# Optimization experiments

Measured on AMD Instinct MI355X. Metric: run time of the kernel, lower is better.

The kernel has to match this reference:

```python
import jax, jax.numpy as jnp
import numpy as np

MU = 0.02
BINS = 30
LOSS_WEIGHT = 1.0
REWEIGHT = 1.0


def setup_inputs() -> dict:
    key = jax.random.key(0)
    k1, k2, k3 = jax.random.split(key, 3)
    B, C = 4194304, 4
    pred = jax.random.normal(k1, (B, C), dtype=jnp.float32)
    target = jax.random.normal(k2, (B, C), dtype=jnp.float32)
    label_weight = jax.random.uniform(k3, (B, C), dtype=jnp.float32)
    return {"pred": pred, "target": target, "label_weight": label_weight}


def reference(pred, target, label_weight):
    mu = jnp.float32(MU)
    diff = pred - target
    # smooth-L1-like (ASL1) loss
    loss = jnp.sqrt(diff * diff + mu * mu) - mu
    # gradient norm g = |d / sqrt(mu^2 + d^2)| in [0, 1); detached in torch
    g = jax.lax.stop_gradient(jnp.abs(diff) * jax.lax.rsqrt(mu * mu + diff * diff))
    valid = label_weight > 0
    # tot comes from .item() in torch -> constant w.r.t. autodiff
    tot = jax.lax.stop_gradient(jnp.maximum(jnp.sum(label_weight), 1.0))
    # edges[i] = i/bins, edges[-1] = 1000 -> bin index = clip(floor(g*bins))
    idx = jnp.clip((g * BINS).astype(jnp.int32), 0, BINS - 1)
    counts = jax.ops.segment_sum(
        valid.astype(jnp.float32).ravel(), idx.ravel(), num_segments=BINS
    )  # [BINS] number of valid samples per gradient-density bin
    n = jnp.sum(counts > 0)  # number of non-empty bins
    weights = jnp.where(valid, tot / jnp.maximum(counts[idx], 1.0), 0.0)
    weights = weights / jnp.maximum(n, 1).astype(jnp.float32)
    weights = jax.lax.stop_gradient(weights)
    loss = jnp.sum(loss * weights * REWEIGHT) / tot
    return loss * LOSS_WEIGHT
```

## Files before the change

kernel.cpp:

```cpp
#include <hip/hip_runtime.h>

#define MU_F    0.02f
#define MU2_F   4.0e-4f
#define TSLOW_F 6.2e-3f
#define BINS    30
#define ROWS    62
#define THREADS 256
#define NBLK    2048

__device__ __forceinline__ void ghmr_elem(float pj, float tj, float wj,
                                          float& sumAll, float& cntAll,
                                          float* s_sum, unsigned int* s_cnt)
{
    float d    = pj - tj;
    float d2   = fmaf(d, d, MU2_F);
    float loss = sqrtf(d2) - MU_F;
    bool valid = wj > 0.0f;
    sumAll += valid ? loss : 0.0f;
    cntAll += valid ? 1.0f : 0.0f;
    if (valid && d2 < TSLOW_F) {
        float g   = fabsf(d) * rsqrtf(d2);
        int   idx = (int)(g * 30.0f);
        idx = idx > BINS - 1 ? BINS - 1 : idx;
        atomicAdd(&s_sum[idx], loss);
        atomicAdd(&s_cnt[idx], 1u);
    }
}

#define GHMR_PROC(P,TT,W) do { \
    ghmr_elem((P).x,(TT).x,(W).x,sumAll,cntAll,s_sum,s_cnt); \
    ghmr_elem((P).y,(TT).y,(W).y,sumAll,cntAll,s_sum,s_cnt); \
    ghmr_elem((P).z,(TT).z,(W).z,sumAll,cntAll,s_sum,s_cnt); \
    ghmr_elem((P).w,(TT).w,(W).w,sumAll,cntAll,s_sum,s_cnt); } while(0)

#define GHMR_TAIL() do { \
    for (int off = 32; off > 0; off >>= 1) { \
        sumAll += __shfl_down(sumAll, off); \
        cntAll += __shfl_down(cntAll, off); \
    } \
    if ((tid & 63) == 0) { atomicAdd(&s_all[0], sumAll); atomicAdd(&s_all[1], cntAll); } \
    __syncthreads(); \
    const int bid = blockIdx.x; \
    if (tid < BINS)            part[tid*pstride + bid] = s_sum[tid]; \
    else if (tid < 2*BINS)     part[tid*pstride + bid] = (float)s_cnt[tid-BINS]; \
    else if (tid == 2*BINS)    part[60*pstride + bid] = s_all[0]; \
    else if (tid == 2*BINS+1)  part[61*pstride + bid] = s_all[1]; } while(0)

__global__ __launch_bounds__(THREADS, 4) void ghmr_hist_chunk(
    const float4* __restrict__ pred, const float4* __restrict__ target,
    const float4* __restrict__ lw, float* __restrict__ part,
    int pstride, int nchunks)
{
    __shared__ float        s_sum[BINS];
    __shared__ unsigned int s_cnt[BINS];
    __shared__ float        s_all[2];

    const int tid = threadIdx.x;
    if (tid < BINS) { s_sum[tid] = 0.0f; s_cnt[tid] = 0u; }
    if (tid < 2)    s_all[tid] = 0.0f;
    __syncthreads();

    float sumAll = 0.0f, cntAll = 0.0f;

    const int G = gridDim.x * THREADS;
    for (int g = blockIdx.x * THREADS + tid; g < nchunks; g += G) {
        const int b = 4 * g;
        float4 p0 = pred[b+0], p1 = pred[b+1], p2 = pred[b+2], p3 = pred[b+3];
        float4 t0 = target[b+0], t1 = target[b+1], t2 = target[b+2], t3 = target[b+3];
        float4 w0 = lw[b+0], w1 = lw[b+1], w2 = lw[b+2], w3 = lw[b+3];
        __builtin_amdgcn_sched_barrier(0);
        GHMR_PROC(p0,t0,w0);
        GHMR_PROC(p1,t1,w1);
        GHMR_PROC(p2,t2,w2);
        GHMR_PROC(p3,t3,w3);
    }

    GHMR_TAIL();
}

__global__ __launch_bounds__(THREADS) void ghmr_hist_gen(
    const float* __restrict__ predf, const float* __restrict__ targetf,
    const float* __restrict__ lwf, float* __restrict__ part,
    int pstride, int n)
{
    __shared__ float        s_sum[BINS];
    __shared__ unsigned int s_cnt[BINS];
    __shared__ float        s_all[2];

    const int tid = threadIdx.x;
    if (tid < BINS) { s_sum[tid] = 0.0f; s_cnt[tid] = 0u; }
    if (tid < 2)    s_all[tid] = 0.0f;
    __syncthreads();

    float sumAll = 0.0f, cntAll = 0.0f;

    const int n4 = n / 4;
    const float4* pred   = (const float4*)predf;
    const float4* target = (const float4*)targetf;
    const float4* lw     = (const float4*)lwf;

    for (int i = blockIdx.x*THREADS + tid; i < n4; i += gridDim.x*THREADS) {
        float4 p = pred[i], t = target[i], w = lw[i];
        GHMR_PROC(p,t,w);
    }
    int rem = n - n4*4;
    if (blockIdx.x == 0 && tid < rem) {
        int i = n4*4 + tid;
        ghmr_elem(predf[i], targetf[i], lwf[i], sumAll, cntAll, s_sum, s_cnt);
    }

    GHMR_TAIL();
}

__global__ __launch_bounds__(256) void ghmr_reduce(
    const float* __restrict__ part, float* __restrict__ red,
    int pstride, int nblk)
{
    const int r = blockIdx.x;
    float s = 0.0f;
    for (int i = threadIdx.x; i < nblk; i += 256)
        s += part[r*pstride + i];
    __shared__ float ls[4];
    for (int off = 32; off > 0; off >>= 1) s += __shfl_down(s, off);
    if ((threadIdx.x & 63) == 0) ls[threadIdx.x >> 6] = s;
    __syncthreads();
    if (threadIdx.x == 0) red[r] = ls[0] + ls[1] + ls[2] + ls[3];
}

__global__ void ghmr_final(const float* __restrict__ red, float* __restrict__ out)
{
    int b = threadIdx.x;
    float Sb = (b < BINS) ? red[b]        : 0.0f;
    float Cb = (b < BINS) ? red[BINS + b] : 0.0f;
    float SS = Sb, CC = Cb;
    for (int off = 1; off < 64; off <<= 1) { SS += __shfl_xor(SS, off); CC += __shfl_xor(CC, off); }
    float SA = red[60], CA = red[61];
    if (b == BINS - 1) { Sb = (SA - SS) + Sb; Cb = (CA - CC) + Cb; }
    float term = (b < BINS) ? Sb / fmaxf(Cb, 1.0f) : 0.0f;
    float nz   = (b < BINS && Cb > 0.0f) ? 1.0f : 0.0f;
    for (int off = 1; off < 64; off <<= 1) { term += __shfl_xor(term, off); nz += __shfl_xor(nz, off); }
    if (b == 0) out[0] = term / fmaxf(nz, 1.0f);
}

extern "C" void kernel_launch(void* const* d_in, const int* in_sizes, int n_in,
                              void* d_out, int out_size, void* d_ws, size_t ws_size,
                              hipStream_t stream) {
    int n = in_sizes[0];

    int NB = NBLK;
    size_t need = (size_t)ROWS * (size_t)NB * sizeof(float) + ROWS * sizeof(float);
    bool ws_ok = need <= ws_size;
    if (!ws_ok) {
        NB = (int)((ws_size / sizeof(float) - ROWS) / ROWS);
        if (NB > NBLK) NB = NBLK;
        if (NB < 1) NB = 1;
    }
    int pstride = NB;
    float* part = (float*)d_ws;
    float* red  = part + (size_t)ROWS * pstride;

    bool fast = ws_ok && (n % 16 == 0) && n > 0;

    if (fast) {
        int nchunks = n / 16;
        ghmr_hist_chunk<<<NB, THREADS, 0, stream>>>(
            (const float4*)d_in[0], (const float4*)d_in[1], (const float4*)d_in[2],
            part, pstride, nchunks);
    } else {
        ghmr_hist_gen<<<NB, THREADS, 0, stream>>>(
            (const float*)d_in[0], (const float*)d_in[1], (const float*)d_in[2],
            part, pstride, n);
    }
    ghmr_reduce<<<ROWS, 256, 0, stream>>>(part, red, pstride, NB);
    ghmr_final<<<1, 64, 0, stream>>>(red, (float*)d_out);
}
```

Before: 44.03 us.

## Double-buffer chunk loads and defer mu subtraction to final reduction

```diff
diff --git a/kernel.cpp b/kernel.cpp
--- a/kernel.cpp
+++ b/kernel.cpp
@@ -9,42 +9,67 @@
 #define NBLK    2048
 
 __device__ __forceinline__ void ghmr_elem(float pj, float tj, float wj,
-                                          float& sumAll, float& cntAll,
+                                          float& sumR, int& cntV,
                                           float* s_sum, unsigned int* s_cnt)
 {
-    float d    = pj - tj;
-    float d2   = fmaf(d, d, MU2_F);
-    float loss = sqrtf(d2) - MU_F;
+    float d  = pj - tj;
+    float d2 = fmaf(d, d, MU2_F);
+    float r  = __builtin_amdgcn_sqrtf(d2);
     bool valid = wj > 0.0f;
-    sumAll += valid ? loss : 0.0f;
-    cntAll += valid ? 1.0f : 0.0f;
+    sumR += valid ? r : 0.0f;
+    cntV += valid ? 1 : 0;
     if (valid && d2 < TSLOW_F) {
-        float g   = fabsf(d) * rsqrtf(d2);
+        float g   = fabsf(d) * __builtin_amdgcn_rsqf(d2);
         int   idx = (int)(g * 30.0f);
         idx = idx > BINS - 1 ? BINS - 1 : idx;
-        atomicAdd(&s_sum[idx], loss);
+        atomicAdd(&s_sum[idx], r);
         atomicAdd(&s_cnt[idx], 1u);
     }
 }
 
+struct Chunk {
+    float4 p0, p1, p2, p3;
+    float4 t0, t1, t2, t3;
+    float4 w0, w1, w2, w3;
+};
+
+__device__ __forceinline__ void load_chunk(Chunk& c,
+    const float4* __restrict__ pred, const float4* __restrict__ target,
+    const float4* __restrict__ lw, int g)
+{
+    const int b = 4 * g;
+    c.p0 = pred[b+0]; c.p1 = pred[b+1]; c.p2 = pred[b+2]; c.p3 = pred[b+3];
+    c.t0 = target[b+0]; c.t1 = target[b+1]; c.t2 = target[b+2]; c.t3 = target[b+3];
+    c.w0 = lw[b+0]; c.w1 = lw[b+1]; c.w2 = lw[b+2]; c.w3 = lw[b+3];
+}
+
 #define GHMR_PROC(P,TT,W) do { \
-    ghmr_elem((P).x,(TT).x,(W).x,sumAll,cntAll,s_sum,s_cnt); \
-    ghmr_elem((P).y,(TT).y,(W).y,sumAll,cntAll,s_sum,s_cnt); \
-    ghmr_elem((P).z,(TT).z,(W).z,sumAll,cntAll,s_sum,s_cnt); \
-    ghmr_elem((P).w,(TT).w,(W).w,sumAll,cntAll,s_sum,s_cnt); } while(0)
+    ghmr_elem((P).x,(TT).x,(W).x,sumR,cntV,s_sum,s_cnt); \
+    ghmr_elem((P).y,(TT).y,(W).y,sumR,cntV,s_sum,s_cnt); \
+    ghmr_elem((P).z,(TT).z,(W).z,sumR,cntV,s_sum,s_cnt); \
+    ghmr_elem((P).w,(TT).w,(W).w,sumR,cntV,s_sum,s_cnt); } while(0)
+
+__device__ __forceinline__ void proc_chunk(const Chunk& c,
+    float& sumR, int& cntV, float* s_sum, unsigned int* s_cnt)
+{
+    GHMR_PROC(c.p0, c.t0, c.w0);
+    GHMR_PROC(c.p1, c.t1, c.w1);
+    GHMR_PROC(c.p2, c.t2, c.w2);
+    GHMR_PROC(c.p3, c.t3, c.w3);
+}
 
 #define GHMR_TAIL() do { \
     for (int off = 32; off > 0; off >>= 1) { \
-        sumAll += __shfl_down(sumAll, off); \
-        cntAll += __shfl_down(cntAll, off); \
+        sumR += __shfl_down(sumR, off); \
+        cntV += __shfl_down(cntV, off); \
     } \
-    if ((tid & 63) == 0) { atomicAdd(&s_all[0], sumAll); atomicAdd(&s_all[1], cntAll); } \
+    if ((tid & 63) == 0) { atomicAdd(&s_allR, sumR); atomicAdd(&s_allC, (unsigned)cntV); } \
     __syncthreads(); \
     const int bid = blockIdx.x; \
     if (tid < BINS)            part[tid*pstride + bid] = s_sum[tid]; \
     else if (tid < 2*BINS)     part[tid*pstride + bid] = (float)s_cnt[tid-BINS]; \
-    else if (tid == 2*BINS)    part[60*pstride + bid] = s_all[0]; \
-    else if (tid == 2*BINS+1)  part[61*pstride + bid] = s_all[1]; } while(0)
+    else if (tid == 2*BINS)    part[60*pstride + bid] = s_allR; \
+    else if (tid == 2*BINS+1)  part[61*pstride + bid] = (float)s_allC; } while(0)
 
 __global__ __launch_bounds__(THREADS, 4) void ghmr_hist_chunk(
     const float4* __restrict__ pred, const float4* __restrict__ target,
@@ -53,26 +78,40 @@
 {
     __shared__ float        s_sum[BINS];
     __shared__ unsigned int s_cnt[BINS];
-    __shared__ float        s_all[2];
+    __shared__ float        s_allR;
+    __shared__ unsigned int s_allC;
 
     const int tid = threadIdx.x;
     if (tid < BINS) { s_sum[tid] = 0.0f; s_cnt[tid] = 0u; }
-    if (tid < 2)    s_all[tid] = 0.0f;
+    if (tid == 0)   { s_allR = 0.0f; s_allC = 0u; }
     __syncthreads();
 
-    float sumAll = 0.0f, cntAll = 0.0f;
+    float sumR = 0.0f;
+    int   cntV = 0;
 
     const int G = gridDim.x * THREADS;
-    for (int g = blockIdx.x * THREADS + tid; g < nchunks; g += G) {
-        const int b = 4 * g;
-        float4 p0 = pred[b+0], p1 = pred[b+1], p2 = pred[b+2], p3 = pred[b+3];
-        float4 t0 = target[b+0], t1 = target[b+1], t2 = target[b+2], t3 = target[b+3];
-        float4 w0 = lw[b+0], w1 = lw[b+1], w2 = lw[b+2], w3 = lw[b+3];
-        __builtin_amdgcn_sched_barrier(0);
-        GHMR_PROC(p0,t0,w0);
-        GHMR_PROC(p1,t1,w1);
-        GHMR_PROC(p2,t2,w2);
-        GHMR_PROC(p3,t3,w3);
+    int g = blockIdx.x * THREADS + tid;
+
+    if (g < nchunks) {
+        Chunk A, B;
+        load_chunk(A, pred, target, lw, g);
+        g += G;
+        bool pendA = true;
+        while (g < nchunks) {
+            if (pendA) {
+                load_chunk(B, pred, target, lw, g);
+                __builtin_amdgcn_sched_barrier(0);
+                proc_chunk(A, sumR, cntV, s_sum, s_cnt);
+            } else {
+                load_chunk(A, pred, target, lw, g);
+                __builtin_amdgcn_sched_barrier(0);
+                proc_chunk(B, sumR, cntV, s_sum, s_cnt);
+            }
+            pendA = !pendA;
+            g += G;
+        }
+        if (pendA) proc_chunk(A, sumR, cntV, s_sum, s_cnt);
+        else       proc_chunk(B, sumR, cntV, s_sum, s_cnt);
     }
 
     GHMR_TAIL();
@@ -85,14 +124,16 @@
 {
     __shared__ float        s_sum[BINS];
     __shared__ unsigned int s_cnt[BINS];
-    __shared__ float        s_all[2];
+    __shared__ float        s_allR;
+    __shared__ unsigned int s_allC;
 
     const int tid = threadIdx.x;
     if (tid < BINS) { s_sum[tid] = 0.0f; s_cnt[tid] = 0u; }
-    if (tid < 2)    s_all[tid] = 0.0f;
+    if (tid == 0)   { s_allR = 0.0f; s_allC = 0u; }
     __syncthreads();
 
-    float sumAll = 0.0f, cntAll = 0.0f;
+    float sumR = 0.0f;
+    int   cntV = 0;
 
     const int n4 = n / 4;
     const float4* pred   = (const float4*)predf;
@@ -106,7 +147,7 @@
     int rem = n - n4*4;
     if (blockIdx.x == 0 && tid < rem) {
         int i = n4*4 + tid;
-        ghmr_elem(predf[i], targetf[i], lwf[i], sumAll, cntAll, s_sum, s_cnt);
+        ghmr_elem(predf[i], targetf[i], lwf[i], sumR, cntV, s_sum, s_cnt);
     }
 
     GHMR_TAIL();
@@ -130,13 +171,13 @@
 __global__ void ghmr_final(const float* __restrict__ red, float* __restrict__ out)
 {
     int b = threadIdx.x;
-    float Sb = (b < BINS) ? red[b]        : 0.0f;
+    float Rb = (b < BINS) ? red[b]        : 0.0f;
     float Cb = (b < BINS) ? red[BINS + b] : 0.0f;
-    float SS = Sb, CC = Cb;
-    for (int off = 1; off < 64; off <<= 1) { SS += __shfl_xor(SS, off); CC += __shfl_xor(CC, off); }
-    float SA = red[60], CA = red[61];
-    if (b == BINS - 1) { Sb = (SA - SS) + Sb; Cb = (CA - CC) + Cb; }
-    float term = (b < BINS) ? Sb / fmaxf(Cb, 1.0f) : 0.0f;
+    float RS = Rb, CS = Cb;
+    for (int off = 1; off < 64; off <<= 1) { RS += __shfl_xor(RS, off); CS += __shfl_xor(CS, off); }
+    float RA = red[60], CA = red[61];
+    if (b == BINS - 1) { Rb = (RA - RS) + Rb; Cb = (CA - CS) + Cb; }
+    float term = (b < BINS) ? (Rb - MU_F * Cb) / fmaxf(Cb, 1.0f) : 0.0f;
     float nz   = (b < BINS && Cb > 0.0f) ? 1.0f : 0.0f;
     for (int off = 1; off < 64; off <<= 1) { term += __shfl_xor(term, off); nz += __shfl_xor(nz, off); }
     if (b == 0) out[0] = term / fmaxf(nz, 1.0f);
```

New measurement: 71.17 us. 1.62x slower.
